# Kernel optimization log

Measured on AMD Instinct MI355X. Metric: run time of the kernel, lower is better.

Reference implementation:

```python
import jax, jax.numpy as jnp
import numpy as np

N_NODES = 50000
N_EDGES = 800000
IN_FEATS = 128
HID_FEATS = 128
NUM_CLASSES = 32


def setup_inputs() -> dict:
    key = jax.random.key(0)
    ks = jax.random.split(key, 7)
    node_embeddings = jax.random.normal(ks[0], (N_NODES, IN_FEATS), jnp.float32)
    edge_encodings = jax.random.normal(ks[1], (N_EDGES, 16), jnp.float32)
    W1 = jax.random.normal(ks[2], (IN_FEATS, HID_FEATS), jnp.float32) / jnp.sqrt(jnp.float32(IN_FEATS))
    b1 = jnp.zeros((HID_FEATS,), jnp.float32)
    W2 = jax.random.normal(ks[3], (HID_FEATS, NUM_CLASSES), jnp.float32) / jnp.sqrt(jnp.float32(HID_FEATS))
    b2 = jnp.zeros((NUM_CLASSES,), jnp.float32)
    edge_index = jax.random.randint(ks[4], (2, N_EDGES), 0, N_NODES, jnp.int32)
    return {"node_embeddings": node_embeddings, "edge_encodings": edge_encodings,
            "W1": W1, "b1": b1, "W2": W2, "b2": b2, "edge_index": edge_index}


def _graph_conv(x, W, b, src, dst, d_out, d_in, n_nodes):
    # DGL GraphConv, norm='both': out = D_in^{-1/2} A D_out^{-1/2} x W + b
    # Apply weight first (out_feats <= in_feats) -- associativity, same math.
    h = (x @ W) * d_out[:, None]            # [N, F_out], source-side norm
    agg = jax.ops.segment_sum(h[src], dst, num_segments=n_nodes)  # SpMM
    return agg * d_in[:, None] + b


def reference(node_embeddings, edge_encodings, W1, b1, W2, b2, edge_index):
    src, dst = edge_index[0], edge_index[1]
    n = node_embeddings.shape[0]
    ones = jnp.ones(src.shape, jnp.float32)
    out_deg = jax.ops.segment_sum(ones, src, num_segments=n)
    in_deg = jax.ops.segment_sum(ones, dst, num_segments=n)
    d_out = jnp.where(out_deg > 0, out_deg, 1.0) ** -0.5
    d_in = jnp.where(in_deg > 0, in_deg, 1.0) ** -0.5
    h = jax.nn.relu(_graph_conv(node_embeddings, W1, b1, src, dst, d_out, d_in, n))
    return _graph_conv(h, W2, b2, src, dst, d_out, d_in, n)
```

## Files before the change

kernel.cpp:

```cpp
#include <hip/hip_runtime.h>


#define F 128
#define C 32
#define PADN 50176
#define SCAN_BLOCKS 49
#define HB 256
#define PADN4 (PADN / 4)

static __device__ __forceinline__ unsigned short bf16_bits(float f) {
    union { float f; unsigned int u; } v; v.f = f;
    unsigned int r = v.u + 0x7fffu + ((v.u >> 16) & 1u);
    return (unsigned short)(r >> 16);
}

__global__ void passA_kernel(const int* __restrict__ dst, int* __restrict__ cnt_in,
                             unsigned short* __restrict__ pos, int E) {
    int e = blockIdx.x * blockDim.x + threadIdx.x;
    if (e >= E) return;
    int p = atomicAdd(&cnt_in[dst[e]], 1);
    pos[e] = (unsigned short)p;
}

__global__ __launch_bounds__(256) void hist_out_kernel(
    const int* __restrict__ src, unsigned int* __restrict__ partial, int E) {
    __shared__ unsigned int h[PADN4];
    const int tid = threadIdx.x;
    for (int j = tid; j < PADN4; j += 256) h[j] = 0u;
    __syncthreads();
    const int per = (E + HB - 1) / HB;
    const int lo = blockIdx.x * per;
    const int hi = min(E, lo + per);
    for (int e = lo + tid; e < hi; e += 256) {
        int v = src[e];
        atomicAdd(&h[v >> 2], 1u << ((v & 3) * 8));
    }
    __syncthreads();
    unsigned int* p = partial + (size_t)blockIdx.x * PADN4;
    for (int j = tid; j < PADN4; j += 256) p[j] = h[j];
}

__global__ void reduce_dinv_kernel(const unsigned int* __restrict__ partial,
                                   const int* __restrict__ cnt_in,
                                   float* __restrict__ dinv_out, float* __restrict__ dinv_in,
                                   int n4) {
    int i = blockIdx.x * blockDim.x + threadIdx.x;
    if (i >= n4) return;
    unsigned int s0 = 0, s1 = 0, s2 = 0, s3 = 0;
#pragma unroll 8
    for (int b = 0; b < HB; ++b) {
        unsigned int w = partial[(size_t)b * PADN4 + i];
        s0 += w & 0xffu; s1 += (w >> 8) & 0xffu; s2 += (w >> 16) & 0xffu; s3 += w >> 24;
    }
    int base = i * 4;
    dinv_out[base + 0] = s0 ? rsqrtf((float)s0) : 1.0f;
    dinv_out[base + 1] = s1 ? rsqrtf((float)s1) : 1.0f;
    dinv_out[base + 2] = s2 ? rsqrtf((float)s2) : 1.0f;
    dinv_out[base + 3] = s3 ? rsqrtf((float)s3) : 1.0f;
    int4 c = *(const int4*)(cnt_in + base);
    dinv_in[base + 0] = c.x > 0 ? rsqrtf((float)c.x) : 1.0f;
    dinv_in[base + 1] = c.y > 0 ? rsqrtf((float)c.y) : 1.0f;
    dinv_in[base + 2] = c.z > 0 ? rsqrtf((float)c.z) : 1.0f;
    dinv_in[base + 3] = c.w > 0 ? rsqrtf((float)c.w) : 1.0f;
}

__global__ __launch_bounds__(256) void scan1_kernel(const int* __restrict__ cnt,
                                                    int* __restrict__ part, int* __restrict__ bsum) {
    __shared__ int sdata[256];
    const int tid = threadIdx.x;
    const int base = blockIdx.x * 1024 + tid * 4;
    int4 c = *(const int4*)(cnt + base);
    int s = c.x + c.y + c.z + c.w;
    sdata[tid] = s;
    __syncthreads();
    for (int off = 1; off < 256; off <<= 1) {
        int v = 0;
        if (tid >= off) v = sdata[tid - off];
        __syncthreads();
        if (tid >= off) sdata[tid] += v;
        __syncthreads();
    }
    int excl = sdata[tid] - s;
    part[base]     = excl;
    part[base + 1] = excl + c.x;
    part[base + 2] = excl + c.x + c.y;
    part[base + 3] = excl + c.x + c.y + c.z;
    if (tid == 255) bsum[blockIdx.x] = sdata[255];
}

__global__ __launch_bounds__(256) void scan2_kernel(int* __restrict__ bsum, int nb) {
    __shared__ int sdata[256];
    const int tid = threadIdx.x;
    int v = (tid < nb) ? bsum[tid] : 0;
    sdata[tid] = v;
    __syncthreads();
    for (int off = 1; off < 256; off <<= 1) {
        int t = 0;
        if (tid >= off) t = sdata[tid - off];
        __syncthreads();
        if (tid >= off) sdata[tid] += t;
        __syncthreads();
    }
    if (tid < nb) bsum[tid] = sdata[tid] - v;
}

__global__ void scan3_kernel(int* __restrict__ row_ptr, const int* __restrict__ bsum, int n) {
    int i = blockIdx.x * blockDim.x + threadIdx.x;
    if (i >= n) return;
    row_ptr[i] += bsum[i >> 10];
}

__global__ void fillB_kernel(const int* __restrict__ src, const int* __restrict__ dst,
                             const unsigned short* __restrict__ pos,
                             const int* __restrict__ row_ptr, int* __restrict__ eidx, int E) {
    int e = blockIdx.x * blockDim.x + threadIdx.x;
    if (e >= E) return;
    eidx[row_ptr[dst[e]] + pos[e]] = src[e];
}

__global__ __launch_bounds__(256) void gemm1_kernel(
    const float* __restrict__ X, const float* __restrict__ W,
    const float* __restrict__ dinv_out, unsigned short* __restrict__ H1, int N) {
    __shared__ float ws[32 * 128];
    __shared__ float xs[32 * 36];
    const int tid = threadIdx.x;
    const int m0 = tid & 15;
    const int rr = tid >> 4;
    const int rbase = blockIdx.x * 32;

    float4 a00 = {0,0,0,0}, a01 = {0,0,0,0}, a10 = {0,0,0,0}, a11 = {0,0,0,0};

    for (int kt = 0; kt < 4; ++kt) {
        const float4* W4 = (const float4*)(W + kt * 32 * 128);
        float4* ws4 = (float4*)ws;
#pragma unroll
        for (int j = 0; j < 4; ++j) ws4[tid + j * 256] = W4[tid + j * 256];
        {
            int r = tid >> 3, k4 = tid & 7;
            int row = rbase + r;
            float4 v = make_float4(0.f, 0.f, 0.f, 0.f);
            if (row < N) v = *(const float4*)(X + (size_t)row * F + kt * 32 + k4 * 4);
            int base = r * 36 + k4 * 4;
            xs[base] = v.x; xs[base + 1] = v.y; xs[base + 2] = v.z; xs[base + 3] = v.w;
        }
        __syncthreads();
#pragma unroll
        for (int kk = 0; kk < 32; ++kk) {
            float xa = xs[(rr * 2) * 36 + kk];
            float xb = xs[(rr * 2 + 1) * 36 + kk];
            float4 wA = *(const float4*)(ws + kk * 128 + m0 * 4);
            float4 wB = *(const float4*)(ws + kk * 128 + 64 + m0 * 4);
            a00.x += xa * wA.x; a00.y += xa * wA.y; a00.z += xa * wA.z; a00.w += xa * wA.w;
            a01.x += xa * wB.x; a01.y += xa * wB.y; a01.z += xa * wB.z; a01.w += xa * wB.w;
            a10.x += xb * wA.x; a10.y += xb * wA.y; a10.z += xb * wA.z; a10.w += xb * wA.w;
            a11.x += xb * wB.x; a11.y += xb * wB.y; a11.z += xb * wB.z; a11.w += xb * wB.w;
        }
        __syncthreads();
    }
    int row0 = rbase + rr * 2;
    int row1 = row0 + 1;
    if (row0 < N) {
        float s = dinv_out[row0];
        ushort4 p0, p1;
        p0.x = bf16_bits(a00.x * s); p0.y = bf16_bits(a00.y * s);
        p0.z = bf16_bits(a00.z * s); p0.w = bf16_bits(a00.w * s);
        p1.x = bf16_bits(a01.x * s); p1.y = bf16_bits(a01.y * s);
        p1.z = bf16_bits(a01.z * s); p1.w = bf16_bits(a01.w * s);
        *(ushort4*)(H1 + (size_t)row0 * F + m0 * 4) = p0;
        *(ushort4*)(H1 + (size_t)row0 * F + 64 + m0 * 4) = p1;
    }
    if (row1 < N) {
        float s = dinv_out[row1];
        ushort4 p0, p1;
        p0.x = bf16_bits(a10.x * s); p0.y = bf16_bits(a10.y * s);
        p0.z = bf16_bits(a10.z * s); p0.w = bf16_bits(a10.w * s);
        p1.x = bf16_bits(a11.x * s); p1.y = bf16_bits(a11.y * s);
        p1.z = bf16_bits(a11.z * s); p1.w = bf16_bits(a11.w * s);
        *(ushort4*)(H1 + (size_t)row1 * F + m0 * 4) = p0;
        *(ushort4*)(H1 + (size_t)row1 * F + 64 + m0 * 4) = p1;
    }
}

__global__ __launch_bounds__(256) void spmm_csr1_kernel(
    const unsigned short* __restrict__ H1, const int* __restrict__ row_ptr,
    const int* __restrict__ cnt, const int* __restrict__ eidx,
    float* __restrict__ AGG1, int N) {
    int node = blockIdx.x * 4 + (threadIdx.x >> 6);
    if (node >= N) return;
    const int l = threadIdx.x & 63;
    const int start = row_ptr[node];
    const int deg = cnt[node];
    const unsigned int* Hb = (const unsigned int*)H1 + l;
    float2 a0 = {0.f,0.f}, a1 = {0.f,0.f}, a2 = {0.f,0.f}, a3 = {0.f,0.f};
    int i = 0;
    for (; i + 3 < deg; i += 4) {
        int s0 = eidx[start + i];
        int s1 = eidx[start + i + 1];
        int s2 = eidx[start + i + 2];
        int s3 = eidx[start + i + 3];
        unsigned int w0 = Hb[(size_t)s0 * 64];
        unsigned int w1 = Hb[(size_t)s1 * 64];
        unsigned int w2 = Hb[(size_t)s2 * 64];
        unsigned int w3 = Hb[(size_t)s3 * 64];
        a0.x += __uint_as_float(w0 << 16); a0.y += __uint_as_float(w0 & 0xffff0000u);
        a1.x += __uint_as_float(w1 << 16); a1.y += __uint_as_float(w1 & 0xffff0000u);
        a2.x += __uint_as_float(w2 << 16); a2.y += __uint_as_float(w2 & 0xffff0000u);
        a3.x += __uint_as_float(w3 << 16); a3.y += __uint_as_float(w3 & 0xffff0000u);
    }
    for (; i < deg; ++i) {
        int s0 = eidx[start + i];
        unsigned int w0 = Hb[(size_t)s0 * 64];
        a0.x += __uint_as_float(w0 << 16); a0.y += __uint_as_float(w0 & 0xffff0000u);
    }
    float2 o = {a0.x + a1.x + a2.x + a3.x, a0.y + a1.y + a2.y + a3.y};
    *(float2*)(AGG1 + (size_t)node * F + l * 2) = o;
}

__global__ __launch_bounds__(256) void gemm2_kernel(
    const float* __restrict__ AGG1, const float* __restrict__ b1,
    const float* __restrict__ dinv_in, const float* __restrict__ W2,
    const float* __restrict__ dinv_out, float* __restrict__ H2, int N) {
    __shared__ float ws[F * C];
    __shared__ float xs[64 * 132];
    const int tid = threadIdx.x;
    const int rbase = blockIdx.x * 64;
    {
        float4* ws4 = (float4*)ws;
        const float4* W4 = (const float4*)W2;
#pragma unroll
        for (int j = 0; j < 4; ++j) ws4[tid + j * 256] = W4[tid + j * 256];
    }
#pragma unroll
    for (int j = 0; j < 8; ++j) {
        int i4 = tid + j * 256;
        int r = i4 >> 5, k4 = i4 & 31;
        int row = rbase + r;
        float4 v = make_float4(0.f, 0.f, 0.f, 0.f);
        float di = 0.f;
        if (row < N) {
            v = *(const float4*)(AGG1 + (size_t)row * F + k4 * 4);
            di = dinv_in[row];
        }
        float4 bb = *(const float4*)(b1 + k4 * 4);
        int base = r * 132 + k4 * 4;
        xs[base]     = fmaxf(fmaf(v.x, di, bb.x), 0.f);
        xs[base + 1] = fmaxf(fmaf(v.y, di, bb.y), 0.f);
        xs[base + 2] = fmaxf(fmaf(v.z, di, bb.z), 0.f);
        xs[base + 3] = fmaxf(fmaf(v.w, di, bb.w), 0.f);
    }
    __syncthreads();
    const int m0 = tid & 7;
    const int rr = tid >> 3;
    float4 a0 = {0,0,0,0}, a1 = {0,0,0,0};
#pragma unroll 8
    for (int k = 0; k < F; ++k) {
        float4 w = *(const float4*)(ws + k * C + m0 * 4);
        float xa = xs[(rr * 2) * 132 + k];
        float xb = xs[(rr * 2 + 1) * 132 + k];
        a0.x += xa * w.x; a0.y += xa * w.y; a0.z += xa * w.z; a0.w += xa * w.w;
        a1.x += xb * w.x; a1.y += xb * w.y; a1.z += xb * w.z; a1.w += xb * w.w;
    }
    int row0 = rbase + rr * 2;
    int row1 = row0 + 1;
    if (row0 < N) {
        float s = dinv_out[row0];
        float4 o = {a0.x * s, a0.y * s, a0.z * s, a0.w * s};
        *(float4*)(H2 + (size_t)row0 * C + m0 * 4) = o;
    }
    if (row1 < N) {
        float s = dinv_out[row1];
        float4 o = {a1.x * s, a1.y * s, a1.z * s, a1.w * s};
        *(float4*)(H2 + (size_t)row1 * C + m0 * 4) = o;
    }
}

__global__ __launch_bounds__(256) void spmm_csr2_kernel(
    const float* __restrict__ H2, const int* __restrict__ row_ptr,
    const int* __restrict__ cnt, const int* __restrict__ eidx,
    const float* __restrict__ dinv_in, const float* __restrict__ b2,
    float* __restrict__ out, int N) {
    int node = blockIdx.x * 8 + (threadIdx.x >> 5);
    if (node >= N) return;
    const int col = threadIdx.x & 31;
    const int start = row_ptr[node];
    const int deg = cnt[node];
    float acc0 = 0.f, acc1 = 0.f;
    int i = 0;
    for (; i + 1 < deg; i += 2) {
        int s0 = eidx[start + i];
        int s1 = eidx[start + i + 1];
        acc0 += H2[(size_t)s0 * C + col];
        acc1 += H2[(size_t)s1 * C + col];
    }
    if (i < deg) acc0 += H2[(size_t)eidx[start + i] * C + col];
    out[(size_t)node * C + col] = fmaf(acc0 + acc1, dinv_in[node], b2[col]);
}

extern "C" void kernel_launch(void* const* d_in, const int* in_sizes, int n_in,
                              void* d_out, int out_size, void* d_ws, size_t ws_size,
                              hipStream_t stream) {
    const float* X  = (const float*)d_in[0];
    const float* W1 = (const float*)d_in[2];
    const float* b1 = (const float*)d_in[3];
    const float* W2 = (const float*)d_in[4];
    const float* b2 = (const float*)d_in[5];
    const int*   ei = (const int*)d_in[6];

    const int N = in_sizes[0] / F;
    const int E = in_sizes[6] / 2;
    const int* src = ei;
    const int* dst = ei + E;

    float* wsf      = (float*)d_ws;
    float* dinv_out = wsf;
    float* dinv_in  = wsf + PADN;
    int* cnt_in  = (int*)(wsf + 2 * PADN);
    int* row_ptr = cnt_in + PADN;
    int* bsum    = row_ptr + PADN;
    unsigned short* pos = (unsigned short*)(bsum + 256);
    int* eidx    = (int*)(pos + E);
    unsigned short* H1 = (unsigned short*)(eidx + E);
    float* AGG1  = (float*)(H1 + (size_t)N * F);
    unsigned int* partial = (unsigned int*)AGG1;
    float* H2    = (float*)H1;
    float* outp  = (float*)d_out;

    hipMemsetAsync(cnt_in, 0, (size_t)PADN * sizeof(int), stream);

    passA_kernel<<<(E + 255) / 256, 256, 0, stream>>>(dst, cnt_in, pos, E);
    hist_out_kernel<<<HB, 256, 0, stream>>>(src, partial, E);
    reduce_dinv_kernel<<<(PADN4 + 255) / 256, 256, 0, stream>>>(partial, cnt_in, dinv_out, dinv_in, PADN4);
    scan1_kernel<<<SCAN_BLOCKS, 256, 0, stream>>>(cnt_in, row_ptr, bsum);
    scan2_kernel<<<1, 256, 0, stream>>>(bsum, SCAN_BLOCKS);
    scan3_kernel<<<PADN / 256, 256, 0, stream>>>(row_ptr, bsum, PADN);
    fillB_kernel<<<(E + 255) / 256, 256, 0, stream>>>(src, dst, pos, row_ptr, eidx, E);

    gemm1_kernel<<<(N + 31) / 32, 256, 0, stream>>>(X, W1, dinv_out, H1, N);
    spmm_csr1_kernel<<<(N + 3) / 4, 256, 0, stream>>>(H1, row_ptr, cnt_in, eidx, AGG1, N);
    gemm2_kernel<<<(N + 63) / 64, 256, 0, stream>>>(AGG1, b1, dinv_in, W2, dinv_out, H2, N);
    spmm_csr2_kernel<<<(N + 7) / 8, 256, 0, stream>>>(H2, row_ptr, cnt_in, eidx, dinv_in, b2, outp, N);
}
```

Baseline: 287.6 us.

## Use bf16 MFMA for first-layer GEMM instead of FP32 FMA tiling

Replaces the FP32 shared-memory-tiled GEMM for X@W1 with a kernel built on 16x16x32 bf16 MFMA instructions. Each block transposes W1 into shared memory as bf16, and each wave computes 16 rows by 128 columns directly from X loaded from global memory and converted to bf16. The aim is to move the dense GEMM onto the matrix cores and cut its ALU time. In exchange, X and W are rounded to bf16 before multiplying, which lowers precision. Every block also redoes the W transpose, and the output stores become scattered 2-byte writes.

```diff
diff --git a/kernel.cpp b/kernel.cpp
--- a/kernel.cpp
+++ b/kernel.cpp
@@ -7,6 +7,9 @@
 #define SCAN_BLOCKS 49
 #define HB 256
 #define PADN4 (PADN / 4)
+
+using bf16x8 = __attribute__((ext_vector_type(8))) short;
+using f32x4  = __attribute__((ext_vector_type(4))) float;
 
 static __device__ __forceinline__ unsigned short bf16_bits(float f) {
     union { float f; unsigned int u; } v; v.f = f;
@@ -118,66 +121,61 @@
     eidx[row_ptr[dst[e]] + pos[e]] = src[e];
 }
 
-__global__ __launch_bounds__(256) void gemm1_kernel(
+__global__ __launch_bounds__(256) void gemm1_mfma_kernel(
     const float* __restrict__ X, const float* __restrict__ W,
     const float* __restrict__ dinv_out, unsigned short* __restrict__ H1, int N) {
-    __shared__ float ws[32 * 128];
-    __shared__ float xs[32 * 36];
-    const int tid = threadIdx.x;
-    const int m0 = tid & 15;
-    const int rr = tid >> 4;
-    const int rbase = blockIdx.x * 32;
-
-    float4 a00 = {0,0,0,0}, a01 = {0,0,0,0}, a10 = {0,0,0,0}, a11 = {0,0,0,0};
-
-    for (int kt = 0; kt < 4; ++kt) {
-        const float4* W4 = (const float4*)(W + kt * 32 * 128);
-        float4* ws4 = (float4*)ws;
-#pragma unroll
-        for (int j = 0; j < 4; ++j) ws4[tid + j * 256] = W4[tid + j * 256];
-        {
-            int r = tid >> 3, k4 = tid & 7;
-            int row = rbase + r;
-            float4 v = make_float4(0.f, 0.f, 0.f, 0.f);
-            if (row < N) v = *(const float4*)(X + (size_t)row * F + kt * 32 + k4 * 4);
-            int base = r * 36 + k4 * 4;
-            xs[base] = v.x; xs[base + 1] = v.y; xs[base + 2] = v.z; xs[base + 3] = v.w;
+    __shared__ unsigned short w1t[128 * 136];
+    const int tid = threadIdx.x;
+#pragma unroll
+    for (int p = 0; p < 16; ++p) {
+        int k = p * 8 + (tid >> 5);
+        int c4 = (tid & 31) * 4;
+        float4 v = *(const float4*)(W + k * 128 + c4);
+        w1t[(c4 + 0) * 136 + k] = bf16_bits(v.x);
+        w1t[(c4 + 1) * 136 + k] = bf16_bits(v.y);
+        w1t[(c4 + 2) * 136 + k] = bf16_bits(v.z);
+        w1t[(c4 + 3) * 136 + k] = bf16_bits(v.w);
+    }
+    __syncthreads();
+
+    const int lane = tid & 63;
+    const int wave = tid >> 6;
+    const int row0 = blockIdx.x * 64 + wave * 16;
+    const int arow = row0 + (lane & 15);
+    const int asrc = (arow < N) ? arow : 0;
+    const int kg = (lane >> 4) * 8;
+
+    f32x4 acc[8];
+#pragma unroll
+    for (int n = 0; n < 8; ++n) acc[n] = (f32x4){0.f, 0.f, 0.f, 0.f};
+
+#pragma unroll
+    for (int kk = 0; kk < 4; ++kk) {
+        const float* xp = X + (size_t)asrc * F + kk * 32 + kg;
+        float4 xa = *(const float4*)(xp);
+        float4 xb = *(const float4*)(xp + 4);
+        bf16x8 a;
+        a[0] = (short)bf16_bits(xa.x); a[1] = (short)bf16_bits(xa.y);
+        a[2] = (short)bf16_bits(xa.z); a[3] = (short)bf16_bits(xa.w);
+        a[4] = (short)bf16_bits(xb.x); a[5] = (short)bf16_bits(xb.y);
+        a[6] = (short)bf16_bits(xb.z); a[7] = (short)bf16_bits(xb.w);
+#pragma unroll
+        for (int n = 0; n < 8; ++n) {
+            const bf16x8 b = *(const bf16x8*)(w1t + (n * 16 + (lane & 15)) * 136 + kk * 32 + kg);
+            acc[n] = __builtin_amdgcn_mfma_f32_16x16x32_bf16(a, b, acc[n], 0, 0, 0);
         }
-        __syncthreads();
-#pragma unroll
-        for (int kk = 0; kk < 32; ++kk) {
-            float xa = xs[(rr * 2) * 36 + kk];
-            float xb = xs[(rr * 2 + 1) * 36 + kk];
-            float4 wA = *(const float4*)(ws + kk * 128 + m0 * 4);
-            float4 wB = *(const float4*)(ws + kk * 128 + 64 + m0 * 4);
-            a00.x += xa * wA.x; a00.y += xa * wA.y; a00.z += xa * wA.z; a00.w += xa * wA.w;
-            a01.x += xa * wB.x; a01.y += xa * wB.y; a01.z += xa * wB.z; a01.w += xa * wB.w;
-            a10.x += xb * wA.x; a10.y += xb * wA.y; a10.z += xb * wA.z; a10.w += xb * wA.w;
-            a11.x += xb * wB.x; a11.y += xb * wB.y; a11.z += xb * wB.z; a11.w += xb * wB.w;
+    }
+
+    const int rbase = row0 + (lane >> 4) * 4;
+#pragma unroll
+    for (int j = 0; j < 4; ++j) {
+        int r = rbase + j;
+        if (r < N) {
+            float s = dinv_out[r];
+            unsigned short* out = H1 + (size_t)r * F + (lane & 15);
+#pragma unroll
+            for (int n = 0; n < 8; ++n) out[n * 16] = bf16_bits(acc[n][j] * s);
         }
-        __syncthreads();
-    }
-    int row0 = rbase + rr * 2;
-    int row1 = row0 + 1;
-    if (row0 < N) {
-        float s = dinv_out[row0];
-        ushort4 p0, p1;
-        p0.x = bf16_bits(a00.x * s); p0.y = bf16_bits(a00.y * s);
-        p0.z = bf16_bits(a00.z * s); p0.w = bf16_bits(a00.w * s);
-        p1.x = bf16_bits(a01.x * s); p1.y = bf16_bits(a01.y * s);
-        p1.z = bf16_bits(a01.z * s); p1.w = bf16_bits(a01.w * s);
-        *(ushort4*)(H1 + (size_t)row0 * F + m0 * 4) = p0;
-        *(ushort4*)(H1 + (size_t)row0 * F + 64 + m0 * 4) = p1;
-    }
-    if (row1 < N) {
-        float s = dinv_out[row1];
-        ushort4 p0, p1;
-        p0.x = bf16_bits(a10.x * s); p0.y = bf16_bits(a10.y * s);
-        p0.z = bf16_bits(a10.z * s); p0.w = bf16_bits(a10.w * s);
-        p1.x = bf16_bits(a11.x * s); p1.y = bf16_bits(a11.y * s);
-        p1.z = bf16_bits(a11.z * s); p1.w = bf16_bits(a11.w * s);
-        *(ushort4*)(H1 + (size_t)row1 * F + m0 * 4) = p0;
-        *(ushort4*)(H1 + (size_t)row1 * F + 64 + m0 * 4) = p1;
     }
 }
 
@@ -335,7 +333,7 @@
     scan3_kernel<<<PADN / 256, 256, 0, stream>>>(row_ptr, bsum, PADN);
     fillB_kernel<<<(E + 255) / 256, 256, 0, stream>>>(src, dst, pos, row_ptr, eidx, E);
 
-    gemm1_kernel<<<(N + 31) / 32, 256, 0, stream>>>(X, W1, dinv_out, H1, N);
+    gemm1_mfma_kernel<<<(N + 63) / 64, 256, 0, stream>>>(X, W1, dinv_out, H1, N);
     spmm_csr1_kernel<<<(N + 3) / 4, 256, 0, stream>>>(H1, row_ptr, cnt_in, eidx, AGG1, N);
     gemm2_kernel<<<(N + 63) / 64, 256, 0, stream>>>(AGG1, b1, dinv_in, W2, dinv_out, H2, N);
     spmm_csr2_kernel<<<(N + 7) / 8, 256, 0, stream>>>(H2, row_ptr, cnt_in, eidx, dinv_in, b2, outp, N);
```

New measurement: 279.4 us. -2.9%, faster.
